# Optimization experiments

Measured on AMD Instinct MI355X. Metric: run time of the kernel, lower is better.

Reference implementation:

```python
import jax, jax.numpy as jnp
import numpy as np

EPS = 1e-6  # flax LayerNorm default

def _layer_norm(x, scale, bias):
    mu = jnp.mean(x, axis=-1, keepdims=True)
    var = jnp.mean(jnp.square(x - mu), axis=-1, keepdims=True)
    return (x - mu) * jax.lax.rsqrt(var + EPS) * scale + bias

def setup_inputs() -> dict:
    key = jax.random.key(0)
    ks = jax.random.split(key, 8)
    B, S, D_in, D_h, D_out, N = 4, 2048, 1024, 2048, 1024, 6
    init = lambda k, shape, fan_in: jax.random.normal(k, shape, jnp.float32) / np.sqrt(fan_in)
    return {
        "x": jax.random.normal(ks[0], (B, S, D_in), jnp.float32),
        "ln1_scale": jnp.ones((D_in,), jnp.float32),
        "ln1_bias": jnp.zeros((D_in,), jnp.float32),
        "w1": init(ks[1], (D_in, D_h), D_in),
        "b1": jnp.zeros((D_h,), jnp.float32),
        "block_ln_scales": jnp.ones((N, D_h), jnp.float32),
        "block_ln_biases": jnp.zeros((N, D_h), jnp.float32),
        "block_ws": init(ks[2], (N, D_h, D_h), D_h),
        "block_bs": jnp.zeros((N, D_h), jnp.float32),
        "ln2_scale": jnp.ones((D_h,), jnp.float32),
        "ln2_bias": jnp.zeros((D_h,), jnp.float32),
        "w2": init(ks[3], (D_h, D_out), D_h),
        "b2": jnp.zeros((D_out,), jnp.float32),
    }

def reference(x, ln1_scale, ln1_bias, w1, b1, block_ln_scales, block_ln_biases,
              block_ws, block_bs, ln2_scale, ln2_bias, w2, b2):
    # stem: LN -> Linear -> SiLU
    h = _layer_norm(x, ln1_scale, ln1_bias)
    h = jax.nn.silu(jnp.einsum('bsd,dh->bsh', h, w1) + b1)

    # residual blocks via scan over stacked params
    def block(h, params):
        s, b, w, lb = params
        y = _layer_norm(h, s, b)
        y = jax.nn.silu(jnp.einsum('bsh,hk->bsk', y, w) + lb)
        return h + y, None

    h, _ = jax.lax.scan(block, h, (block_ln_scales, block_ln_biases, block_ws, block_bs))

    # head: LN -> Linear
    h = _layer_norm(h, ln2_scale, ln2_bias)
    return jnp.einsum('bsh,ho->bso', h, w2) + b2
```

## Files before the change

### kernel.cpp

```cpp
#include <hip/hip_runtime.h>
#include <hip/hip_bf16.h>

typedef short short8 __attribute__((ext_vector_type(8)));
typedef float f32x4 __attribute__((ext_vector_type(4)));

#define AS1(p) ((const __attribute__((address_space(1))) void*)(p))
#define AS3(p) ((__attribute__((address_space(3))) void*)(p))

__device__ __forceinline__ ushort f2bf(float f) {
  __hip_bfloat16 h = __float2bfloat16(f);
  return *reinterpret_cast<const ushort*>(&h);
}
__device__ __forceinline__ float bfu2f(ushort u) {
  unsigned int x = ((unsigned int)u) << 16;
  float f;
  __builtin_memcpy(&f, &x, 4);
  return f;
}
__device__ __forceinline__ float silu_f(float v) { return v / (1.f + __expf(-v)); }

template<int NV>
__global__ __launch_bounds__(256) void ln_bf16_k(
    const float* __restrict__ in, const float* __restrict__ sc,
    const float* __restrict__ bi, ushort* __restrict__ out)
{
  const int D = NV * 1024;
  const long row = blockIdx.x;
  const int tx = threadIdx.x;
  const float* p = in + row * (long)D;
  float4 v[NV];
  float s = 0.f, s2 = 0.f;
#pragma unroll
  for (int t = 0; t < NV; ++t) {
    v[t] = *reinterpret_cast<const float4*>(p + t * 1024 + tx * 4);
    s  += v[t].x + v[t].y + v[t].z + v[t].w;
    s2 += v[t].x * v[t].x + v[t].y * v[t].y + v[t].z * v[t].z + v[t].w * v[t].w;
  }
#pragma unroll
  for (int o = 1; o < 64; o <<= 1) { s += __shfl_xor(s, o); s2 += __shfl_xor(s2, o); }
  __shared__ float red[2][4];
  const int wave = tx >> 6;
  if ((tx & 63) == 0) { red[0][wave] = s; red[1][wave] = s2; }
  __syncthreads();
  s  = red[0][0] + red[0][1] + red[0][2] + red[0][3];
  s2 = red[1][0] + red[1][1] + red[1][2] + red[1][3];
  const float mu   = s / D;
  const float rstd = rsqrtf(s2 / D - mu * mu + 1e-6f);
#pragma unroll
  for (int t = 0; t < NV; ++t) {
    const int d = t * 1024 + tx * 4;
    float4 g = *reinterpret_cast<const float4*>(sc + d);
    float4 b = *reinterpret_cast<const float4*>(bi + d);
    ushort4 o;
    o.x = f2bf((v[t].x - mu) * rstd * g.x + b.x);
    o.y = f2bf((v[t].y - mu) * rstd * g.y + b.y);
    o.z = f2bf((v[t].z - mu) * rstd * g.z + b.z);
    o.w = f2bf((v[t].w - mu) * rstd * g.w + b.w);
    *reinterpret_cast<ushort4*>(out + row * (long)D + d) = o;
  }
}

__global__ __launch_bounds__(256) void ln_stats_k(
    const ushort* __restrict__ in, float2* __restrict__ stats)
{
  const long row = blockIdx.x;
  const int tx = threadIdx.x;
  short8 v8 = *reinterpret_cast<const short8*>(in + row * 2048 + tx * 8);
  float s = 0.f, s2 = 0.f;
#pragma unroll
  for (int j = 0; j < 8; ++j) {
    const float v = bfu2f((ushort)v8[j]);
    s += v; s2 += v * v;
  }
#pragma unroll
  for (int o = 1; o < 64; o <<= 1) { s += __shfl_xor(s, o); s2 += __shfl_xor(s2, o); }
  __shared__ float red[2][4];
  const int wave = tx >> 6;
  if ((tx & 63) == 0) { red[0][wave] = s; red[1][wave] = s2; }
  __syncthreads();
  if (tx == 0) {
    s  = red[0][0] + red[0][1] + red[0][2] + red[0][3];
    s2 = red[1][0] + red[1][1] + red[1][2] + red[1][3];
    const float mu   = s * (1.f / 2048.f);
    const float rstd = rsqrtf(s2 * (1.f / 2048.f) - mu * mu + 1e-6f);
    stats[row] = make_float2(mu * rstd, rstd);
  }
}

__global__ __launch_bounds__(256) void transpose_bf16_k(
    const float* __restrict__ in, ushort* __restrict__ out, int K, int N)
{
  __shared__ float tile[64][65];
  const int k0 = blockIdx.y * 64, n0 = blockIdx.x * 64;
  const int tx = threadIdx.x, ty = threadIdx.y;
#pragma unroll
  for (int r = ty; r < 64; r += 4)
    tile[r][tx] = in[(long)(k0 + r) * N + n0 + tx];
  __syncthreads();
#pragma unroll
  for (int r = ty; r < 64; r += 4)
    out[(long)(n0 + r) * K + k0 + tx] = f2bf(tile[tx][r]);
}

__global__ __launch_bounds__(256) void transpose_scale_k(
    const float* __restrict__ in, const float* __restrict__ g,
    const float* __restrict__ beta, ushort* __restrict__ out,
    float2* __restrict__ uvw, int K, int N)
{
  __shared__ float tile[64][65];
  const int k0 = blockIdx.y * 64, n0 = blockIdx.x * 64;
  const int tx = threadIdx.x, ty = threadIdx.y;
  float pu = 0.f, pv = 0.f;
#pragma unroll
  for (int r = ty; r < 64; r += 4) {
    const float w  = in[(long)(k0 + r) * N + n0 + tx];
    const float ws = g[k0 + r] * w;
    tile[r][tx] = ws;
    pu += ws;
    pv += beta[k0 + r] * w;
  }
  atomicAdd(&uvw[n0 + tx].x, pu);
  atomicAdd(&uvw[n0 + tx].y, pv);
  __syncthreads();
#pragma unroll
  for (int r = ty; r < 64; r += 4)
    out[(long)(n0 + r) * K + k0 + tx] = f2bf(tile[tx][r]);
}

#define STG(gsrc, ldst)                                                          \
  __builtin_amdgcn_global_load_lds(AS1(gsrc),          AS3(ldst),          16, 0, 0); \
  __builtin_amdgcn_global_load_lds(AS1((gsrc) + offQ), AS3((ldst) + 8192), 16, 0, 0)

#define ldsA(B, H) (ldsW + (B) * 65536 + (H) * 16384)
#define ldsB(B, H) (ldsW + (B) * 65536 + 32768 + (H) * 16384)

#define RD_AF(DST, DB, MH, KS)                                                  \
  _Pragma("unroll") for (int i_ = 0; i_ < 4; ++i_)                              \
    DST[i_] = *(const short8*)(smem + (DB) * 65536 + aOff + ((MH) * 4 + i_) * 2048 + rdk[(KS)])

#define RD_BF(DST, DB, KS)                                                      \
  _Pragma("unroll") for (int j_ = 0; j_ < 4; ++j_)                              \
    DST[j_] = *(const short8*)(smem + (DB) * 65536 + bOff + j_ * 2048 + rdk[(KS)])

#define MFMA16(AREG, MH, BREG)                                                  \
  _Pragma("unroll") for (int i_ = 0; i_ < 4; ++i_)                              \
  _Pragma("unroll") for (int j_ = 0; j_ < 4; ++j_)                              \
    acc[(MH) * 4 + i_][j_] = __builtin_amdgcn_mfma_f32_16x16x32_bf16(           \
        AREG[i_], BREG[j_], acc[(MH) * 4 + i_][j_], 0, 0, 0)

#define BARRIER __builtin_amdgcn_s_barrier()
#define SP1 __builtin_amdgcn_s_setprio(1)
#define SP0 __builtin_amdgcn_s_setprio(0)
#define SBAR __builtin_amdgcn_sched_barrier(0)
#define LGKMW(N) do { asm volatile("s_waitcnt lgkmcnt(" #N ")"); SBAR; } while (0)
#define W4 do { asm volatile("s_waitcnt vmcnt(4)" ::: "memory"); SBAR; } while (0)
#define W0 do { asm volatile("s_waitcnt vmcnt(0)" ::: "memory"); SBAR; } while (0)
#define WN do {} while (0)

#define DO_TILE(DB, S1, AO, S2, BO, WAITE)                                      \
             \
  RD_AF(afx, DB, 0, 0);                                                         \
  RD_BF(bf, DB, 0);                                                             \
  RD_AF(afy, DB, 1, 0);                                                         \
  if (S1) { STG(aP + (AO), ldsA((DB) ^ 1, 0));                                  \
            STG(aP + (AO) + offH, ldsA((DB) ^ 1, 1)); }                         \
  LGKMW(4);                                     \
  SP1; MFMA16(afx, 0, bf); SP0;                                                 \
                  \
  RD_AF(afx, DB, 0, 1);                                                         \
  LGKMW(4);                                      \
  SP1; MFMA16(afy, 1, bf); SP0;                                                 \
  RD_BF(bf, DB, 1);                                                             \
  SBAR;                                                                         \
                                 \
  RD_AF(afy, DB, 1, 1);                                                         \
  LGKMW(4);                                     \
  SP1; MFMA16(afx, 0, bf); SP0;                                                 \
  BARRIER;                                         \
                  \
  if (S2) { STG(bP + (BO), ldsB(DB, 0));                                        \
            STG(bP + (BO) + offH, ldsB(DB, 1)); }                               \
  LGKMW(0);                                                                     \
  SP1; MFMA16(afy, 1, bf); SP0;                                                 \
  WAITE;                                                                        \
  BARRIER;

template<int MODE>
__global__ __launch_bounds__(512, 2) void gemm256_k(
    const ushort* __restrict__ A, const ushort* __restrict__ Bt,
    const float* __restrict__ bias, const float2* __restrict__ stats,
    const float2* __restrict__ uvw, const ushort* __restrict__ Rin,
    void* __restrict__ Cv, int M, int N, int K)
{
  extern __shared__ char smem[];
  const int tid = threadIdx.x;
  const int lane = tid & 63, wid = tid >> 6;
  const int wr = wid >> 2, wc = wid & 3;
  const int nbx = N >> 8;

  int bid;
  {
    const int b = blockIdx.x;
    const int cpx = gridDim.x >> 3;
    bid = (b & 7) * cpx + (b >> 3);
  }
  const int bx = bid % nbx, by = bid / nbx;
  const long m0 = (long)by << 8, n0 = (long)bx << 8;

  const int srow = tid >> 3;
  const int scol = (((tid & 7) * 16) ^ (((tid >> 3) & 7) << 4)) >> 1;
  const ushort* aP = A  + (m0 + srow) * (long)K + scol;
  const ushort* bP = Bt + (n0 + srow) * (long)K + scol;
  const long offH = 128L * K, offQ = 64L * K;
  char* ldsW = smem + wid * 1024;

  int rdk[2];
  rdk[0] = (((lane >> 4) * 16)     ) ^ ((lane & 7) << 4);
  rdk[1] = (((lane >> 4) * 16) + 64) ^ ((lane & 7) << 4);
  const int aOff = wr * 16384 + (lane & 15) * 128;
  const int bOff = 32768 + (wc >> 1) * 16384 + ((wc & 1) * 64 + (lane & 15)) * 128;

  f32x4 acc[8][4] = {};
  const int NT = K >> 6;

  STG(aP,      ldsA(0, 0));  STG(aP + offH,      ldsA(0, 1));
  STG(bP,      ldsB(0, 0));  STG(bP + offH,      ldsB(0, 1));
  STG(bP + 64, ldsB(1, 0));  STG(bP + 64 + offH, ldsB(1, 1));
  W4;
  BARRIER;

  short8 afx[4], afy[4], bf[4];
  for (int t = 0; t < NT - 2; t += 2) {
    DO_TILE(0, 1,  64, 1, 128, W4)
    DO_TILE(1, 1, 128, 1, 192, W4)
    aP += 128; bP += 128;
  }
  DO_TILE(0, 1, 64, 0, 0, W0)
  DO_TILE(1, 0,  0, 0, 0, WN)

  if (MODE == 0) {
#pragma unroll
    for (int j = 0; j < 4; ++j) {
      const long col = n0 + wc * 64 + j * 16 + (lane & 15);
      const float bj = bias[col];
#pragma unroll
      for (int i = 0; i < 8; ++i) {
        const long rowb = m0 + wr * 128 + i * 16 + ((lane >> 4) << 2);
#pragma unroll
        for (int r = 0; r < 4; ++r) {
          const float v = acc[i][j][r] + bj;
          ((ushort*)Cv)[(rowb + r) * N + col] = f2bf(silu_f(v));
        }
      }
    }
  } else {
    float2 uvv[4];
    float  bj4[4];
    long   col4[4];
#pragma unroll
    for (int j = 0; j < 4; ++j) {
      col4[j] = n0 + wc * 64 + j * 16 + (lane & 15);
      uvv[j]  = uvw[col4[j]];
      bj4[j]  = bias[col4[j]];
    }
#pragma unroll
    for (int i = 0; i < 8; ++i) {
      const long rowb = m0 + wr * 128 + i * 16 + ((lane >> 4) << 2);
#pragma unroll
      for (int r = 0; r < 4; ++r) {
        const long row = rowb + r;
        const float2 ms = stats[row];
#pragma unroll
        for (int j = 0; j < 4; ++j) {
          const float v = ms.y * acc[i][j][r] - ms.x * uvv[j].x + uvv[j].y + bj4[j];
          const long idx = row * N + col4[j];
          if (MODE == 3) {
            ((ushort*)Cv)[idx] = f2bf(bfu2f(Rin[idx]) + silu_f(v));
          } else {
            ((float*)Cv)[idx] = v;
          }
        }
      }
    }
  }
}

extern "C" void kernel_launch(void* const* d_in, const int* in_sizes, int n_in,
                              void* d_out, int out_size, void* d_ws, size_t ws_size,
                              hipStream_t stream) {
  const float* x     = (const float*)d_in[0];
  const float* ln1_s = (const float*)d_in[1];
  const float* ln1_b = (const float*)d_in[2];
  const float* w1    = (const float*)d_in[3];
  const float* b1    = (const float*)d_in[4];
  const float* bln_s = (const float*)d_in[5];
  const float* bln_b = (const float*)d_in[6];
  const float* bws   = (const float*)d_in[7];
  const float* bbs   = (const float*)d_in[8];
  const float* ln2_s = (const float*)d_in[9];
  const float* ln2_b = (const float*)d_in[10];
  const float* w2    = (const float*)d_in[11];
  const float* b2    = (const float*)d_in[12];
  float* out = (float*)d_out;

  const int M = 8192;
  char* ws = (char*)d_ws;
  ushort* h0   = (ushort*)ws;
  ushort* h1   = (ushort*)(ws + 33554432);
  ushort* Abf  = h1;
  ushort* wt   = (ushort*)(ws + 67108864);
  float2* uvw  = (float2*)(ws + 125829120);
  float2* stats = (float2*)(ws + 125829120 + 114688);
  const long W1T = 0;
  const long BLK = 2097152;
  const long W2T = BLK + 6L * 4194304;

  (void)hipFuncSetAttribute((const void*)gemm256_k<0>,
      hipFuncAttributeMaxDynamicSharedMemorySize, 131072);
  (void)hipFuncSetAttribute((const void*)gemm256_k<3>,
      hipFuncAttributeMaxDynamicSharedMemorySize, 131072);
  (void)hipFuncSetAttribute((const void*)gemm256_k<4>,
      hipFuncAttributeMaxDynamicSharedMemorySize, 131072);

  (void)hipMemsetAsync(uvw, 0, 7 * 2048 * sizeof(float2), stream);

  dim3 tb(64, 4);
  transpose_bf16_k<<<dim3(32, 16), tb, 0, stream>>>(w1, wt + W1T, 1024, 2048);
  for (int i = 0; i < 6; ++i)
    transpose_scale_k<<<dim3(32, 32), tb, 0, stream>>>(
        bws + (long)i * 2048 * 2048, bln_s + i * 2048, bln_b + i * 2048,
        wt + BLK + (long)i * 4194304, uvw + (long)i * 2048, 2048, 2048);
  transpose_scale_k<<<dim3(16, 32), tb, 0, stream>>>(
      w2, ln2_s, ln2_b, wt + W2T, uvw + 6L * 2048, 2048, 1024);

  ln_bf16_k<1><<<M, 256, 0, stream>>>(x, ln1_s, ln1_b, Abf);
  gemm256_k<0><<<32 * 8, 512, 131072, stream>>>(
      Abf, wt + W1T, b1, nullptr, nullptr, nullptr, (void*)h0, M, 2048, 1024);

  ushort* hin = h0;
  ushort* hout = h1;
  for (int i = 0; i < 6; ++i) {
    ln_stats_k<<<M, 256, 0, stream>>>(hin, stats);
    gemm256_k<3><<<32 * 8, 512, 131072, stream>>>(
        hin, wt + BLK + (long)i * 4194304, bbs + i * 2048, stats,
        uvw + (long)i * 2048, hin, (void*)hout, M, 2048, 2048);
    ushort* tmp = hin; hin = hout; hout = tmp;
  }

  ln_stats_k<<<M, 256, 0, stream>>>(hin, stats);
  gemm256_k<4><<<32 * 4, 512, 131072, stream>>>(
      hin, wt + W2T, b2, stats, uvw + 6L * 2048, nullptr, (void*)out, M, 1024, 2048);
}
```

Measured before the change: 693.1 us.

## Fuse LayerNorm row statistics into GEMM epilogues and split-K the head GEMM

Removes the separate ln_stats kernels. Each GEMM epilogue now accumulates per-row sum and sum-of-squares of its output into a buffer using atomics, and the next GEMM derives mean and rstd from those sums. The head GEMM is split over K into two halves whose results are atomically added into a zeroed output, to raise block count. It also changes the B prologue loads to direct global-to-LDS loads with separate leading dimensions. The cost is extra atomics and memsets, and sums are taken from float values before bf16 rounding, which can slightly change the statistics.

```diff
diff --git a/kernel.cpp b/kernel.cpp
--- a/kernel.cpp
+++ b/kernel.cpp
@@ -60,33 +60,6 @@
   }
 }
 
-__global__ __launch_bounds__(256) void ln_stats_k(
-    const ushort* __restrict__ in, float2* __restrict__ stats)
-{
-  const long row = blockIdx.x;
-  const int tx = threadIdx.x;
-  short8 v8 = *reinterpret_cast<const short8*>(in + row * 2048 + tx * 8);
-  float s = 0.f, s2 = 0.f;
-#pragma unroll
-  for (int j = 0; j < 8; ++j) {
-    const float v = bfu2f((ushort)v8[j]);
-    s += v; s2 += v * v;
-  }
-#pragma unroll
-  for (int o = 1; o < 64; o <<= 1) { s += __shfl_xor(s, o); s2 += __shfl_xor(s2, o); }
-  __shared__ float red[2][4];
-  const int wave = tx >> 6;
-  if ((tx & 63) == 0) { red[0][wave] = s; red[1][wave] = s2; }
-  __syncthreads();
-  if (tx == 0) {
-    s  = red[0][0] + red[0][1] + red[0][2] + red[0][3];
-    s2 = red[1][0] + red[1][1] + red[1][2] + red[1][3];
-    const float mu   = s * (1.f / 2048.f);
-    const float rstd = rsqrtf(s2 * (1.f / 2048.f) - mu * mu + 1e-6f);
-    stats[row] = make_float2(mu * rstd, rstd);
-  }
-}
-
 __global__ __launch_bounds__(256) void transpose_bf16_k(
     const float* __restrict__ in, ushort* __restrict__ out, int K, int N)
 {
@@ -158,26 +131,22 @@
 #define WN do {} while (0)
 
 #define DO_TILE(DB, S1, AO, S2, BO, WAITE)                                      \
-             \
   RD_AF(afx, DB, 0, 0);                                                         \
   RD_BF(bf, DB, 0);                                                             \
   RD_AF(afy, DB, 1, 0);                                                         \
   if (S1) { STG(aP + (AO), ldsA((DB) ^ 1, 0));                                  \
             STG(aP + (AO) + offH, ldsA((DB) ^ 1, 1)); }                         \
-  LGKMW(4);                                     \
+  LGKMW(4);                                                                     \
   SP1; MFMA16(afx, 0, bf); SP0;                                                 \
-                  \
   RD_AF(afx, DB, 0, 1);                                                         \
-  LGKMW(4);                                      \
+  LGKMW(4);                                                                     \
   SP1; MFMA16(afy, 1, bf); SP0;                                                 \
   RD_BF(bf, DB, 1);                                                             \
   SBAR;                                                                         \
-                                 \
   RD_AF(afy, DB, 1, 1);                                                         \
-  LGKMW(4);                                     \
+  LGKMW(4);                                                                     \
   SP1; MFMA16(afx, 0, bf); SP0;                                                 \
-  BARRIER;                                         \
-                  \
+  BARRIER;                                                                      \
   if (S2) { STG(bP + (BO), ldsB(DB, 0));                                        \
             STG(bP + (BO) + offH, ldsB(DB, 1)); }                               \
   LGKMW(0);                                                                     \
@@ -188,9 +157,10 @@
 template<int MODE>
 __global__ __launch_bounds__(512, 2) void gemm256_k(
     const ushort* __restrict__ A, const ushort* __restrict__ Bt,
-    const float* __restrict__ bias, const float2* __restrict__ stats,
+    const float* __restrict__ bias, const float2* __restrict__ sumsIn,
     const float2* __restrict__ uvw, const ushort* __restrict__ Rin,
-    void* __restrict__ Cv, int M, int N, int K)
+    float2* __restrict__ sumsOut, void* __restrict__ Cv,
+    int M, int N, int K, int ldA, int ldB)
 {
   extern __shared__ char smem[];
   const int tid = threadIdx.x;
@@ -204,14 +174,18 @@
     const int cpx = gridDim.x >> 3;
     bid = (b & 7) * cpx + (b >> 3);
   }
+  int kb = 0;
+  if (MODE == 5) { kb = bid >> 7; bid &= 127; }
   const int bx = bid % nbx, by = bid / nbx;
   const long m0 = (long)by << 8, n0 = (long)bx << 8;
 
   const int srow = tid >> 3;
   const int scol = (((tid & 7) * 16) ^ (((tid >> 3) & 7) << 4)) >> 1;
-  const ushort* aP = A  + (m0 + srow) * (long)K + scol;
-  const ushort* bP = Bt + (n0 + srow) * (long)K + scol;
-  const long offH = 128L * K, offQ = 64L * K;
+  const ushort* aP = A  + (long)kb * 1024 + (m0 + srow) * (long)ldA + scol;
+  const ushort* bP = Bt + (long)kb * 1024 + (n0 + srow) * (long)ldB + scol;
+  const long offH = 128L * ldA;
+  const long offQ = 64L * ldA;
+  const long offHB = 128L * ldB, offQB = 64L * ldB;
   char* ldsW = smem + wid * 1024;
 
   int rdk[2];
@@ -223,13 +197,25 @@
   f32x4 acc[8][4] = {};
   const int NT = K >> 6;
 
-  STG(aP,      ldsA(0, 0));  STG(aP + offH,      ldsA(0, 1));
-  STG(bP,      ldsB(0, 0));  STG(bP + offH,      ldsB(0, 1));
-  STG(bP + 64, ldsB(1, 0));  STG(bP + 64 + offH, ldsB(1, 1));
+  STG(aP, ldsA(0, 0));
+  STG(aP + offH, ldsA(0, 1));
+  {
+    const long offQ_save = offQ; (void)offQ_save;
+  }
+  __builtin_amdgcn_global_load_lds(AS1(bP),                AS3(ldsB(0, 0)),        16, 0, 0);
+  __builtin_amdgcn_global_load_lds(AS1(bP + offQB),        AS3(ldsB(0, 0) + 8192), 16, 0, 0);
+  __builtin_amdgcn_global_load_lds(AS1(bP + offHB),        AS3(ldsB(0, 1)),        16, 0, 0);
+  __builtin_amdgcn_global_load_lds(AS1(bP + offHB + offQB),AS3(ldsB(0, 1) + 8192), 16, 0, 0);
+  __builtin_amdgcn_global_load_lds(AS1(bP + 64),                AS3(ldsB(1, 0)),        16, 0, 0);
+  __builtin_amdgcn_global_load_lds(AS1(bP + 64 + offQB),        AS3(ldsB(1, 0) + 8192), 16, 0, 0);
+  __builtin_amdgcn_global_load_lds(AS1(bP + 64 + offHB),        AS3(ldsB(1, 1)),        16, 0, 0);
+  __builtin_amdgcn_global_load_lds(AS1(bP + 64 + offHB + offQB),AS3(ldsB(1, 1) + 8192), 16, 0, 0);
   W4;
   BARRIER;
 
   short8 afx[4], afy[4], bf[4];
+  {
+  }
   for (int t = 0; t < NT - 2; t += 2) {
     DO_TILE(0, 1,  64, 1, 128, W4)
     DO_TILE(1, 1, 128, 1, 192, W4)
@@ -238,47 +224,57 @@
   DO_TILE(0, 1, 64, 0, 0, W0)
   DO_TILE(1, 0,  0, 0, 0, WN)
 
-  if (MODE == 0) {
-#pragma unroll
-    for (int j = 0; j < 4; ++j) {
-      const long col = n0 + wc * 64 + j * 16 + (lane & 15);
-      const float bj = bias[col];
-#pragma unroll
-      for (int i = 0; i < 8; ++i) {
-        const long rowb = m0 + wr * 128 + i * 16 + ((lane >> 4) << 2);
-#pragma unroll
-        for (int r = 0; r < 4; ++r) {
-          const float v = acc[i][j][r] + bj;
-          ((ushort*)Cv)[(rowb + r) * N + col] = f2bf(silu_f(v));
+  const float cw = (MODE == 5 && kb != 0) ? 0.f : 1.f;
+  long  col4[4];
+  float bj4[4];
+  float2 uvv[4];
+#pragma unroll
+  for (int j = 0; j < 4; ++j) {
+    col4[j] = n0 + wc * 64 + j * 16 + (lane & 15);
+    bj4[j]  = bias[col4[j]];
+    if (MODE != 0) uvv[j] = uvw[col4[j]];
+  }
+#pragma unroll
+  for (int i = 0; i < 8; ++i) {
+#pragma unroll
+    for (int r = 0; r < 4; ++r) {
+      const long row = m0 + wr * 128 + i * 16 + ((lane >> 4) << 2) + r;
+      float mu_rstd = 0.f, rstd = 1.f;
+      if (MODE != 0) {
+        const float2 ss = sumsIn[row];
+        const float mu = ss.x * (1.f / 2048.f);
+        rstd = rsqrtf(ss.y * (1.f / 2048.f) - mu * mu + 1e-6f);
+        mu_rstd = mu * rstd;
+      }
+      float ps = 0.f, ps2 = 0.f;
+#pragma unroll
+      for (int j = 0; j < 4; ++j) {
+        const long idx = row * (long)N + col4[j];
+        if (MODE == 0) {
+          const float hv = silu_f(acc[i][j][r] + bj4[j]);
+          ((ushort*)Cv)[idx] = f2bf(hv);
+          ps += hv; ps2 += hv * hv;
+        } else if (MODE == 3) {
+          const float v = rstd * acc[i][j][r] - mu_rstd * uvv[j].x + uvv[j].y + bj4[j];
+          const float hv = bfu2f(Rin[idx]) + silu_f(v);
+          ((ushort*)Cv)[idx] = f2bf(hv);
+          ps += hv; ps2 += hv * hv;
+        } else {
+          const float v = rstd * acc[i][j][r]
+                        + cw * (uvv[j].y + bj4[j] - mu_rstd * uvv[j].x);
+          unsafeAtomicAdd(&((float*)Cv)[idx], v);
         }
       }
-    }
-  } else {
-    float2 uvv[4];
-    float  bj4[4];
-    long   col4[4];
-#pragma unroll
-    for (int j = 0; j < 4; ++j) {
-      col4[j] = n0 + wc * 64 + j * 16 + (lane & 15);
-      uvv[j]  = uvw[col4[j]];
-      bj4[j]  = bias[col4[j]];
-    }
-#pragma unroll
-    for (int i = 0; i < 8; ++i) {
-      const long rowb = m0 + wr * 128 + i * 16 + ((lane >> 4) << 2);
-#pragma unroll
-      for (int r = 0; r < 4; ++r) {
-        const long row = rowb + r;
-        const float2 ms = stats[row];
-#pragma unroll
-        for (int j = 0; j < 4; ++j) {
-          const float v = ms.y * acc[i][j][r] - ms.x * uvv[j].x + uvv[j].y + bj4[j];
-          const long idx = row * N + col4[j];
-          if (MODE == 3) {
-            ((ushort*)Cv)[idx] = f2bf(bfu2f(Rin[idx]) + silu_f(v));
-          } else {
-            ((float*)Cv)[idx] = v;
-          }
+      if (MODE == 0 || MODE == 3) {
+#pragma unroll
+        for (int o = 1; o < 16; o <<= 1) {
+          ps  += __shfl_xor(ps, o);
+          ps2 += __shfl_xor(ps2, o);
+        }
+        if ((lane & 15) == 0) {
+          float* sp = (float*)(sumsOut + row);
+          unsafeAtomicAdd(sp, ps);
+          unsafeAtomicAdd(sp + 1, ps2);
         }
       }
     }
@@ -305,12 +301,12 @@
 
   const int M = 8192;
   char* ws = (char*)d_ws;
-  ushort* h0   = (ushort*)ws;
-  ushort* h1   = (ushort*)(ws + 33554432);
-  ushort* Abf  = h1;
-  ushort* wt   = (ushort*)(ws + 67108864);
-  float2* uvw  = (float2*)(ws + 125829120);
-  float2* stats = (float2*)(ws + 125829120 + 114688);
+  ushort* h0    = (ushort*)ws;
+  ushort* h1    = (ushort*)(ws + 33554432);
+  ushort* Abf   = h1;
+  ushort* wt    = (ushort*)(ws + 67108864);
+  float2* uvw   = (float2*)(ws + 125829120);
+  float2* sums  = (float2*)(ws + 125829120 + 131072);
   const long W1T = 0;
   const long BLK = 2097152;
   const long W2T = BLK + 6L * 4194304;
@@ -319,10 +315,12 @@
       hipFuncAttributeMaxDynamicSharedMemorySize, 131072);
   (void)hipFuncSetAttribute((const void*)gemm256_k<3>,
       hipFuncAttributeMaxDynamicSharedMemorySize, 131072);
-  (void)hipFuncSetAttribute((const void*)gemm256_k<4>,
+  (void)hipFuncSetAttribute((const void*)gemm256_k<5>,
       hipFuncAttributeMaxDynamicSharedMemorySize, 131072);
 
   (void)hipMemsetAsync(uvw, 0, 7 * 2048 * sizeof(float2), stream);
+  (void)hipMemsetAsync(sums, 0, 7 * 8192 * sizeof(float2), stream);
+  (void)hipMemsetAsync(out, 0, (size_t)M * 1024 * sizeof(float), stream);
 
   dim3 tb(64, 4);
   transpose_bf16_k<<<dim3(32, 16), tb, 0, stream>>>(w1, wt + W1T, 1024, 2048);
@@ -335,19 +333,20 @@
 
   ln_bf16_k<1><<<M, 256, 0, stream>>>(x, ln1_s, ln1_b, Abf);
   gemm256_k<0><<<32 * 8, 512, 131072, stream>>>(
-      Abf, wt + W1T, b1, nullptr, nullptr, nullptr, (void*)h0, M, 2048, 1024);
+      Abf, wt + W1T, b1, nullptr, nullptr, nullptr, sums,
+      (void*)h0, M, 2048, 1024, 1024, 1024);
 
   ushort* hin = h0;
   ushort* hout = h1;
   for (int i = 0; i < 6; ++i) {
-    ln_stats_k<<<M, 256, 0, stream>>>(hin, stats);
     gemm256_k<3><<<32 * 8, 512, 131072, stream>>>(
-        hin, wt + BLK + (long)i * 4194304, bbs + i * 2048, stats,
-        uvw + (long)i * 2048, hin, (void*)hout, M, 2048, 2048);
+        hin, wt + BLK + (long)i * 4194304, bbs + i * 2048,
+        sums + (long)i * 8192, uvw + (long)i * 2048, hin,
+        sums + (long)(i + 1) * 8192, (void*)hout, M, 2048, 2048, 2048, 2048);
     ushort* tmp = hin; hin = hout; hout = tmp;
   }
 
-  ln_stats_k<<<M, 256, 0, stream>>>(hin, stats);
-  gemm256_k<4><<<32 * 4, 512, 131072, stream>>>(
-      hin, wt + W2T, b2, stats, uvw + 6L * 2048, nullptr, (void*)out, M, 1024, 2048);
-}
+  gemm256_k<5><<<32 * 4 * 2, 512, 131072, stream>>>(
+      hin, wt + W2T, b2, sums + 6L * 8192, uvw + 6L * 2048, nullptr,
+      nullptr, (void*)out, M, 1024, 1024, 2048, 2048);
+}
```

Result: slower. 800.5 us (+15.5%).

## Split-K the head GEMM across two halves and batch block weight transposes

Applied to the files above, without the earlier changes.

The final head GEMM (N=1024) launched only 128 workgroups, so it is now split along K into two halves. That gives 256 workgroups, with the second half writing raw partial sums to a scratch buffer and a combine kernel adding them into the output. The six per-block weight transpose launches are also merged into one launch using blockIdx.z. The cost is an extra fp32 partial-buffer round trip and one more kernel launch.

```diff
diff --git a/kernel.cpp b/kernel.cpp
--- a/kernel.cpp
+++ b/kernel.cpp
@@ -103,11 +103,17 @@
 }
 
 __global__ __launch_bounds__(256) void transpose_scale_k(
-    const float* __restrict__ in, const float* __restrict__ g,
-    const float* __restrict__ beta, ushort* __restrict__ out,
-    float2* __restrict__ uvw, int K, int N)
+    const float* __restrict__ in0, const float* __restrict__ g0,
+    const float* __restrict__ beta0, ushort* __restrict__ out0,
+    float2* __restrict__ uvw0, int K, int N)
 {
   __shared__ float tile[64][65];
+  const int z = blockIdx.z;
+  const float* in    = in0 + (long)z * K * N;
+  const float* g     = g0 + (long)z * K;
+  const float* beta  = beta0 + (long)z * K;
+  ushort* out        = out0 + (long)z * K * N;
+  float2* uvw        = uvw0 + (long)z * N;
   const int k0 = blockIdx.y * 64, n0 = blockIdx.x * 64;
   const int tx = threadIdx.x, ty = threadIdx.y;
   float pu = 0.f, pv = 0.f;
@@ -125,6 +131,16 @@
 #pragma unroll
   for (int r = ty; r < 64; r += 4)
     out[(long)(n0 + r) * K + k0 + tx] = f2bf(tile[tx][r]);
+}
+
+__global__ __launch_bounds__(512) void combine_k(
+    float* __restrict__ out, const float* __restrict__ part)
+{
+  const long i = ((long)blockIdx.x * 512 + threadIdx.x) * 4;
+  float4 a = *reinterpret_cast<const float4*>(out + i);
+  float4 b = *reinterpret_cast<const float4*>(part + i);
+  a.x += b.x; a.y += b.y; a.z += b.z; a.w += b.w;
+  *reinterpret_cast<float4*>(out + i) = a;
 }
 
 #define STG(gsrc, ldst)                                                          \
@@ -158,26 +174,22 @@
 #define WN do {} while (0)
 
 #define DO_TILE(DB, S1, AO, S2, BO, WAITE)                                      \
-             \
   RD_AF(afx, DB, 0, 0);                                                         \
   RD_BF(bf, DB, 0);                                                             \
   RD_AF(afy, DB, 1, 0);                                                         \
   if (S1) { STG(aP + (AO), ldsA((DB) ^ 1, 0));                                  \
             STG(aP + (AO) + offH, ldsA((DB) ^ 1, 1)); }                         \
-  LGKMW(4);                                     \
+  LGKMW(4);                                                                     \
   SP1; MFMA16(afx, 0, bf); SP0;                                                 \
-                  \
   RD_AF(afx, DB, 0, 1);                                                         \
-  LGKMW(4);                                      \
+  LGKMW(4);                                                                     \
   SP1; MFMA16(afy, 1, bf); SP0;                                                 \
   RD_BF(bf, DB, 1);                                                             \
   SBAR;                                                                         \
-                                 \
   RD_AF(afy, DB, 1, 1);                                                         \
-  LGKMW(4);                                     \
+  LGKMW(4);                                                                     \
   SP1; MFMA16(afx, 0, bf); SP0;                                                 \
-  BARRIER;                                         \
-                  \
+  BARRIER;                                                                      \
   if (S2) { STG(bP + (BO), ldsB(DB, 0));                                        \
             STG(bP + (BO) + offH, ldsB(DB, 1)); }                               \
   LGKMW(0);                                                                     \
@@ -190,7 +202,8 @@
     const ushort* __restrict__ A, const ushort* __restrict__ Bt,
     const float* __restrict__ bias, const float2* __restrict__ stats,
     const float2* __restrict__ uvw, const ushort* __restrict__ Rin,
-    void* __restrict__ Cv, int M, int N, int K)
+    void* __restrict__ Cv, float* __restrict__ Cv2,
+    int M, int N, int K, int ld)
 {
   extern __shared__ char smem[];
   const int tid = threadIdx.x;
@@ -204,14 +217,16 @@
     const int cpx = gridDim.x >> 3;
     bid = (b & 7) * cpx + (b >> 3);
   }
+  int kb = 0;
+  if (MODE == 5) { kb = bid >> 7; bid &= 127; }
   const int bx = bid % nbx, by = bid / nbx;
   const long m0 = (long)by << 8, n0 = (long)bx << 8;
 
   const int srow = tid >> 3;
   const int scol = (((tid & 7) * 16) ^ (((tid >> 3) & 7) << 4)) >> 1;
-  const ushort* aP = A  + (m0 + srow) * (long)K + scol;
-  const ushort* bP = Bt + (n0 + srow) * (long)K + scol;
-  const long offH = 128L * K, offQ = 64L * K;
+  const ushort* aP = A  + (long)kb * 1024 + (m0 + srow) * (long)ld + scol;
+  const ushort* bP = Bt + (long)kb * 1024 + (n0 + srow) * (long)ld + scol;
+  const long offH = 128L * ld, offQ = 64L * ld;
   char* ldsW = smem + wid * 1024;
 
   int rdk[2];
@@ -263,6 +278,8 @@
       uvv[j]  = uvw[col4[j]];
       bj4[j]  = bias[col4[j]];
     }
+    float* dst = (MODE == 5 && kb == 1) ? Cv2 : (float*)Cv;
+    const float cw = (MODE == 5 && kb == 1) ? 0.f : 1.f;
 #pragma unroll
     for (int i = 0; i < 8; ++i) {
       const long rowb = m0 + wr * 128 + i * 16 + ((lane >> 4) << 2);
@@ -272,12 +289,14 @@
         const float2 ms = stats[row];
 #pragma unroll
         for (int j = 0; j < 4; ++j) {
-          const float v = ms.y * acc[i][j][r] - ms.x * uvv[j].x + uvv[j].y + bj4[j];
-          const long idx = row * N + col4[j];
+          const long idx = row * (long)N + col4[j];
           if (MODE == 3) {
+            const float v = ms.y * acc[i][j][r] - ms.x * uvv[j].x + uvv[j].y + bj4[j];
             ((ushort*)Cv)[idx] = f2bf(bfu2f(Rin[idx]) + silu_f(v));
           } else {
-            ((float*)Cv)[idx] = v;
+            const float v = ms.y * acc[i][j][r]
+                          + cw * (uvv[j].y + bj4[j] - ms.x * uvv[j].x);
+            dst[idx] = v;
           }
         }
       }
@@ -305,12 +324,12 @@
 
   const int M = 8192;
   char* ws = (char*)d_ws;
-  ushort* h0   = (ushort*)ws;
-  ushort* h1   = (ushort*)(ws + 33554432);
-  ushort* Abf  = h1;
-  ushort* wt   = (ushort*)(ws + 67108864);
-  float2* uvw  = (float2*)(ws + 125829120);
-  float2* stats = (float2*)(ws + 125829120 + 114688);
+  ushort* h0    = (ushort*)ws;
+  ushort* h1    = (ushort*)(ws + 33554432);
+  ushort* Abf   = h1;
+  ushort* wt    = (ushort*)(ws + 67108864);
+  float2* uvw   = (float2*)(ws + 125829120);
+  float2* stats = (float2*)(ws + 125829120 + 131072);
   const long W1T = 0;
   const long BLK = 2097152;
   const long W2T = BLK + 6L * 4194304;
@@ -319,23 +338,22 @@
       hipFuncAttributeMaxDynamicSharedMemorySize, 131072);
   (void)hipFuncSetAttribute((const void*)gemm256_k<3>,
       hipFuncAttributeMaxDynamicSharedMemorySize, 131072);
-  (void)hipFuncSetAttribute((const void*)gemm256_k<4>,
+  (void)hipFuncSetAttribute((const void*)gemm256_k<5>,
       hipFuncAttributeMaxDynamicSharedMemorySize, 131072);
 
   (void)hipMemsetAsync(uvw, 0, 7 * 2048 * sizeof(float2), stream);
 
   dim3 tb(64, 4);
   transpose_bf16_k<<<dim3(32, 16), tb, 0, stream>>>(w1, wt + W1T, 1024, 2048);
-  for (int i = 0; i < 6; ++i)
-    transpose_scale_k<<<dim3(32, 32), tb, 0, stream>>>(
-        bws + (long)i * 2048 * 2048, bln_s + i * 2048, bln_b + i * 2048,
-        wt + BLK + (long)i * 4194304, uvw + (long)i * 2048, 2048, 2048);
-  transpose_scale_k<<<dim3(16, 32), tb, 0, stream>>>(
+  transpose_scale_k<<<dim3(32, 32, 6), tb, 0, stream>>>(
+      bws, bln_s, bln_b, wt + BLK, uvw, 2048, 2048);
+  transpose_scale_k<<<dim3(16, 32, 1), tb, 0, stream>>>(
       w2, ln2_s, ln2_b, wt + W2T, uvw + 6L * 2048, 2048, 1024);
 
   ln_bf16_k<1><<<M, 256, 0, stream>>>(x, ln1_s, ln1_b, Abf);
   gemm256_k<0><<<32 * 8, 512, 131072, stream>>>(
-      Abf, wt + W1T, b1, nullptr, nullptr, nullptr, (void*)h0, M, 2048, 1024);
+      Abf, wt + W1T, b1, nullptr, nullptr, nullptr,
+      (void*)h0, nullptr, M, 2048, 1024, 1024);
 
   ushort* hin = h0;
   ushort* hout = h1;
@@ -343,11 +361,14 @@
     ln_stats_k<<<M, 256, 0, stream>>>(hin, stats);
     gemm256_k<3><<<32 * 8, 512, 131072, stream>>>(
         hin, wt + BLK + (long)i * 4194304, bbs + i * 2048, stats,
-        uvw + (long)i * 2048, hin, (void*)hout, M, 2048, 2048);
+        uvw + (long)i * 2048, hin, (void*)hout, nullptr, M, 2048, 2048, 2048);
     ushort* tmp = hin; hin = hout; hout = tmp;
   }
 
+  float* part = (float*)h1;
   ln_stats_k<<<M, 256, 0, stream>>>(hin, stats);
-  gemm256_k<4><<<32 * 4, 512, 131072, stream>>>(
-      hin, wt + W2T, b2, stats, uvw + 6L * 2048, nullptr, (void*)out, M, 1024, 2048);
-}
+  gemm256_k<5><<<32 * 4 * 2, 512, 131072, stream>>>(
+      hin, wt + W2T, b2, stats, uvw + 6L * 2048, nullptr,
+      (void*)out, part, M, 1024, 1024, 2048);
+  combine_k<<<4096, 512, 0, stream>>>(out, part);
+}
```

Measured after the change: 650.4 us. 6.2% less time.
